# Performance work log

Hardware: AMD Instinct MI355X
Metric: run time of the kernel (lower is better)

## Reference

```python
import jax, jax.numpy as jnp
import numpy as np

B, H, P, L = 8, 512, 512, 2048
HIGH_STAB, LOW_STAB = 0.9, 0.99  # 0 <= high < |lambda| <= low <= 1 (discrete dynamics)


def setup_inputs() -> dict:
    key = jax.random.key(0)
    k_u, k_mag, k_ph, k_b, k_c, k_d = jax.random.split(key, 6)
    u = jax.random.normal(k_u, (B, H, L), dtype=jnp.float32)
    # Frozen diagonal reservoir state matrix Lambda_bar: complex eigenvalues with
    # magnitude in (high_stability, low_stability], random phase (stored as real/imag pairs).
    mag = jax.random.uniform(k_mag, (P,), minval=HIGH_STAB, maxval=LOW_STAB)
    phase = jax.random.uniform(k_ph, (P,), minval=0.0, maxval=2.0 * np.pi)
    Lambda_bar_ri = jnp.stack([mag * jnp.cos(phase), mag * jnp.sin(phase)], axis=-1)  # (P,2)
    B_bar_ri = jax.random.normal(k_b, (P, H, 2), dtype=jnp.float32)  # complex B_bar as real pairs
    C_ri = jax.random.normal(k_c, (H, P, 2), dtype=jnp.float32)      # complex C as real pairs
    D = jax.random.normal(k_d, (H, H), dtype=jnp.float32)
    return {"u": u, "Lambda_bar_ri": Lambda_bar_ri, "B_bar_ri": B_bar_ri, "C_ri": C_ri, "D": D}


def _binary_op(e_i, e_j):
    A_i, Bu_i = e_i
    A_j, Bu_j = e_j
    return (A_j * A_i, A_j * Bu_i + Bu_j)


def reference(u, Lambda_bar_ri, B_bar_ri, C_ri, D):
    Lam = jax.lax.complex(Lambda_bar_ri[:, 0], Lambda_bar_ri[:, 1])        # (P,)
    B_bar = jax.lax.complex(B_bar_ri[..., 0], B_bar_ri[..., 1])            # (P,H)
    C = jax.lax.complex(C_ri[..., 0], C_ri[..., 1])                        # (H,P)
    # Bu_t = B_bar @ u_t for all t, batched: (B,P,L) complex
    Bu = jnp.einsum('ph,bhl->bpl', B_bar, u.astype(B_bar.dtype))
    A = jnp.broadcast_to(Lam[None, :, None], Bu.shape)                     # (B,P,L)
    # Parallel associative scan: x_t = Lam * x_{t-1} + Bu_t
    _, x = jax.lax.associative_scan(_binary_op, (A, Bu), axis=2)           # (B,P,L)
    C_A_Bu = jnp.einsum('hp,bpl->bhl', C, x).real                          # (B,H,L)
    # torch.einsum('hh,bhl->bhl', D, u) uses only the diagonal of D
    Du = jnp.diagonal(D)[None, :, None] * u
    return jax.nn.gelu(C_A_Bu + Du, approximate=False)
```

## Files before the change

### kernel.cpp

```cpp
#include <hip/hip_runtime.h>
#include <cstdint>
#include <cstddef>

#define BB 8
#define HH 512
#define PP 512
#define LL 2048

typedef __attribute__((ext_vector_type(8))) __bf16 bf16x8;
typedef __attribute__((ext_vector_type(4))) float f32x4;

__device__ __forceinline__ uint16_t f2bf(float f) {
  uint32_t u = __builtin_bit_cast(uint32_t, f);
  u += 0x7FFFu + ((u >> 16) & 1u);
  return (uint16_t)(u >> 16);
}

__device__ __forceinline__ void async_copy16(const void* gptr, void* ldsptr) {
  __builtin_amdgcn_global_load_lds(
      (const __attribute__((address_space(1))) unsigned int*)gptr,
      (__attribute__((address_space(3))) unsigned int*)ldsptr,
      16, 0, 0);
}

__global__ __launch_bounds__(256) void prep_and_transpose(
    const float* __restrict__ U, const float* __restrict__ Bbar,
    const float* __restrict__ Cri, const float* __restrict__ Dm,
    uint16_t* __restrict__ Ut, uint16_t* __restrict__ A1,
    uint16_t* __restrict__ A2, float* __restrict__ Dd) {
  __shared__ uint16_t tile[64][66];
  const int t = threadIdx.x;
  if (blockIdx.x < 2048) {
    const int bid = blockIdx.x;
    const int b = bid >> 8;
    const int h0 = ((bid >> 5) & 7) * 64;
    const int l0 = (bid & 31) * 64;
    const int r = t >> 2, c = t & 3;
    const float* src = U + ((size_t)(b * 512 + h0 + r)) * 2048 + l0 + c * 16;
#pragma unroll
    for (int q = 0; q < 4; ++q) {
      float4 v = *(const float4*)(src + q * 4);
      *(uint32_t*)&tile[r][c * 16 + q * 4]     = (uint32_t)f2bf(v.x) | ((uint32_t)f2bf(v.y) << 16);
      *(uint32_t*)&tile[r][c * 16 + q * 4 + 2] = (uint32_t)f2bf(v.z) | ((uint32_t)f2bf(v.w) << 16);
    }
    __syncthreads();
    uint16_t* dst = Ut + ((size_t)(b * 2048 + l0 + r)) * 512 + h0 + c * 16;
    uint32_t o[8];
#pragma unroll
    for (int k = 0; k < 8; ++k)
      o[k] = (uint32_t)tile[c * 16 + 2 * k][r] | ((uint32_t)tile[c * 16 + 2 * k + 1][r] << 16);
    *(uint4*)(dst)     = make_uint4(o[0], o[1], o[2], o[3]);
    *(uint4*)(dst + 8) = make_uint4(o[4], o[5], o[6], o[7]);
  } else {
    int idx = (blockIdx.x - 2048) * 256 + t;
    int p = idx >> 9, h = idx & 511;
    A1[(size_t)p * 512 + h]          = f2bf(Bbar[((size_t)p * 512 + h) * 2 + 0]);
    A1[(size_t)(512 + p) * 512 + h]  = f2bf(Bbar[((size_t)p * 512 + h) * 2 + 1]);
    int h2 = idx >> 9, p2 = idx & 511;
    A2[(size_t)h2 * 1024 + p2]        = f2bf( Cri[((size_t)h2 * 512 + p2) * 2 + 0]);
    A2[(size_t)h2 * 1024 + 512 + p2]  = f2bf(-Cri[((size_t)h2 * 512 + p2) * 2 + 1]);
    if (idx < 512) Dd[idx] = Dm[(size_t)idx * 512 + idx];
  }
}

__global__ __launch_bounds__(512) void scan_tr(
    const float* __restrict__ Lam, const uint16_t* __restrict__ Bu,
    uint16_t* __restrict__ Xt8) {
  __shared__ uint16_t S[16][2048];
  const int t = threadIdx.x, wave = t >> 6, lane = t & 63;
  const int b = blockIdx.x >> 6, p0 = (blockIdx.x & 63) * 8, p = p0 + wave;

  const float lr = Lam[p * 2 + 0], li = Lam[p * 2 + 1];
  float ar = lr, ai = li;
#pragma unroll
  for (int s = 0; s < 5; ++s) { float nr = ar * ar - ai * ai, ni = 2.f * ar * ai; ar = nr; ai = ni; }

  const uint16_t* rowre = Bu + ((size_t)(b * 1024 + p)) * 2048 + lane * 32;
  const uint16_t* rowim = Bu + ((size_t)(b * 1024 + 512 + p)) * 2048 + lane * 32;
  uint4 vr[4], vi[4];
#pragma unroll
  for (int q = 0; q < 4; ++q) { vr[q] = ((const uint4*)rowre)[q]; vi[q] = ((const uint4*)rowim)[q]; }

  float xr[32], xi[32];
  float sr = 0.f, si = 0.f;
#pragma unroll
  for (int q = 0; q < 4; ++q) {
    uint32_t wr[4] = {vr[q].x, vr[q].y, vr[q].z, vr[q].w};
    uint32_t wi[4] = {vi[q].x, vi[q].y, vi[q].z, vi[q].w};
#pragma unroll
    for (int d = 0; d < 4; ++d) {
      float br0 = __builtin_bit_cast(float, wr[d] << 16);
      float bi0 = __builtin_bit_cast(float, wi[d] << 16);
      float br1 = __builtin_bit_cast(float, wr[d] & 0xFFFF0000u);
      float bi1 = __builtin_bit_cast(float, wi[d] & 0xFFFF0000u);
      int j = q * 8 + d * 2;
      float nr = lr * sr - li * si + br0, ni = lr * si + li * sr + bi0;
      sr = nr; si = ni; xr[j] = sr; xi[j] = si;
      nr = lr * sr - li * si + br1; ni = lr * si + li * sr + bi1;
      sr = nr; si = ni; xr[j + 1] = sr; xi[j + 1] = si;
    }
  }
  float Ar = ar, Ai = ai, Sr = sr, Si = si;
#pragma unroll
  for (int off = 1; off < 64; off <<= 1) {
    float pAr = __shfl_up(Ar, off), pAi = __shfl_up(Ai, off);
    float pSr = __shfl_up(Sr, off), pSi = __shfl_up(Si, off);
    if (lane >= off) {
      float tSr = Ar * pSr - Ai * pSi + Sr;
      float tSi = Ar * pSi + Ai * pSr + Si;
      float tAr = Ar * pAr - Ai * pAi;
      float tAi = Ar * pAi + Ai * pAr;
      Sr = tSr; Si = tSi; Ar = tAr; Ai = tAi;
    }
  }
  float Cr = __shfl_up(Sr, 1), Ci = __shfl_up(Si, 1);
  if (lane == 0) { Cr = 0.f; Ci = 0.f; }
  float fr_ = lr * Cr - li * Ci, fi_ = lr * Ci + li * Cr;
#pragma unroll
  for (int j = 0; j < 32; ++j) {
    xr[j] += fr_; xi[j] += fi_;
    float nfr = fr_ * lr - fi_ * li, nfi = fr_ * li + fi_ * lr;
    fr_ = nfr; fi_ = nfi;
  }
  const int wsw = (lane & 7) << 3;
#pragma unroll
  for (int q = 0; q < 4; ++q) {
    uint32_t wr[4], wi[4];
#pragma unroll
    for (int d = 0; d < 4; ++d) {
      int j = q * 8 + d * 2;
      wr[d] = (uint32_t)f2bf(xr[j]) | ((uint32_t)f2bf(xr[j + 1]) << 16);
      wi[d] = (uint32_t)f2bf(xi[j]) | ((uint32_t)f2bf(xi[j + 1]) << 16);
    }
    const int col = (lane * 32 + q * 8) ^ wsw;
    *(uint4*)&S[wave * 2 + 0][col] = make_uint4(wr[0], wr[1], wr[2], wr[3]);
    *(uint4*)&S[wave * 2 + 1][col] = make_uint4(wi[0], wi[1], wi[2], wi[3]);
  }
  __syncthreads();
  const size_t gre = (size_t)b * 128 + (p0 >> 3);
#pragma unroll
  for (int c = 0; c < 2; ++c) {
    uint16_t* dst = Xt8 + (gre + (size_t)c * 64) * 2048 * 8;
#pragma unroll
    for (int rep = 0; rep < 4; ++rep) {
      int l = rep * 512 + t;
      int ls = l ^ (((l >> 5) & 7) << 3);
      uint32_t o0 = (uint32_t)S[0 + c][ls] | ((uint32_t)S[2 + c][ls] << 16);
      uint32_t o1 = (uint32_t)S[4 + c][ls] | ((uint32_t)S[6 + c][ls] << 16);
      uint32_t o2 = (uint32_t)S[8 + c][ls] | ((uint32_t)S[10 + c][ls] << 16);
      uint32_t o3 = (uint32_t)S[12 + c][ls] | ((uint32_t)S[14 + c][ls] << 16);
      *(uint4*)(dst + (size_t)l * 8) = make_uint4(o0, o1, o2, o3);
    }
  }
}

#define GEMM_CORE(KDIM, PB0_EXPR, BSTRIDE)                                    \
  constexpr int K = (KDIM), NT = K / 32;                                      \
  __shared__ __align__(16) uint16_t Alds[2][128 * 32];                        \
  __shared__ __align__(16) uint16_t Blds[2][64 * 32];                         \
  const int t = threadIdx.x, lane = t & 63, w = t >> 6;                       \
  const int m0 = blockIdx.y * 128, n0 = blockIdx.x * 64, b = blockIdx.z;      \
  const int r0 = t >> 2;                                                      \
  const int c0 = (t & 3) ^ ((r0 >> 1) & 3);                                   \
  const uint16_t* pA0 = Amat + (size_t)(m0 + r0) * K + c0 * 8;                \
  const uint16_t* pA1 = Amat + (size_t)(m0 + 64 + r0) * K + c0 * 8;           \
  const uint16_t* pB0 = (PB0_EXPR);                                           \
  const int d0 = t * 8;                                                       \
  const int wm = (w >> 1) * 64, wn = (w & 1) * 32;                            \
  const int fr = lane & 15, fq = lane >> 4;                                   \
  int offA[4], offB[2];                                                       \
  _Pragma("unroll")                                                           \
  for (int i = 0; i < 4; ++i) {                                               \
    int rm = wm + i * 16 + fr;                                                \
    offA[i] = rm * 32 + ((fq ^ ((rm >> 1) & 3)) * 8);                         \
  }                                                                           \
  _Pragma("unroll")                                                           \
  for (int j = 0; j < 2; ++j) {                                               \
    int rn = wn + j * 16 + fr;                                                \
    offB[j] = rn * 32 + ((fq ^ ((rn >> 1) & 3)) * 8);                         \
  }                                                                           \
  f32x4 acc[4][2];                                                            \
  _Pragma("unroll")                                                           \
  for (int i = 0; i < 4; ++i)                                                 \
    _Pragma("unroll")                                                         \
    for (int j = 0; j < 2; ++j) acc[i][j] = (f32x4){0.f, 0.f, 0.f, 0.f};      \
  async_copy16(pA0, &Alds[0][d0]);                                            \
  async_copy16(pA1, &Alds[0][2048 + d0]);                                     \
  async_copy16(pB0, &Blds[0][d0]);                                            \
  __syncthreads();                                                            \
  _Pragma("unroll 2")                                                         \
  for (int it = 0; it < NT; ++it) {                                           \
    const int cur = it & 1, nxt = cur ^ 1;                                    \
    if (it + 1 < NT) {                                                        \
      const int kb = (it + 1) * 32;                                           \
      async_copy16(pA0 + kb, &Alds[nxt][d0]);                                 \
      async_copy16(pA1 + kb, &Alds[nxt][2048 + d0]);                          \
      async_copy16(pB0 + (size_t)(it + 1) * (BSTRIDE), &Blds[nxt][d0]);       \
    }                                                                         \
    bf16x8 af[4], bv[2];                                                      \
    _Pragma("unroll")                                                         \
    for (int i = 0; i < 4; ++i) af[i] = *(const bf16x8*)&Alds[cur][offA[i]];  \
    _Pragma("unroll")                                                         \
    for (int j = 0; j < 2; ++j) bv[j] = *(const bf16x8*)&Blds[cur][offB[j]];  \
    _Pragma("unroll")                                                         \
    for (int i = 0; i < 4; ++i)                                               \
      _Pragma("unroll")                                                       \
      for (int j = 0; j < 2; ++j)                                             \
        acc[i][j] = __builtin_amdgcn_mfma_f32_16x16x32_bf16(af[i], bv[j], acc[i][j], 0, 0, 0); \
    __syncthreads();                                                          \
  }

__global__ __launch_bounds__(256) void gemm1_fused(
    const uint16_t* __restrict__ Amat, const uint16_t* __restrict__ Bt,
    uint16_t* __restrict__ Bu) {
  GEMM_CORE(512, Bt + ((size_t)b * 2048 + n0 + r0) * 512 + c0 * 8, 32)
  uint16_t* O = Bu + ((size_t)b * 1024 + m0) * 2048 + n0;
#pragma unroll
  for (int i = 0; i < 4; ++i)
#pragma unroll
    for (int j = 0; j < 2; ++j)
#pragma unroll
      for (int r = 0; r < 4; ++r) {
        int mm = wm + i * 16 + fq * 4 + r;
        int nn = wn + j * 16 + fr;
        O[(size_t)mm * 2048 + nn] = f2bf(acc[i][j][r]);
      }
}

__global__ __launch_bounds__(256) void gemm2_fused(
    const uint16_t* __restrict__ Amat, const uint16_t* __restrict__ Bt,
    float* __restrict__ Out, const float* __restrict__ Dd,
    const float* __restrict__ Uu) {
  GEMM_CORE(1024, Bt + (((size_t)b * 128 + c0) * 2048 + n0 + r0) * 8, 65536)
  const size_t base = ((size_t)b * 512 + m0) * 2048 + n0;
  float* O = Out + base;
  const float* Ub = Uu + base;
#pragma unroll
  for (int i = 0; i < 4; ++i)
#pragma unroll
    for (int r = 0; r < 4; ++r) {
      int mm = wm + i * 16 + fq * 4 + r;
      float dv = Dd[m0 + mm];
#pragma unroll
      for (int j = 0; j < 2; ++j) {
        int nn = wn + j * 16 + fr;
        float xv = acc[i][j][r] + dv * Ub[(size_t)mm * 2048 + nn];
        O[(size_t)mm * 2048 + nn] = 0.5f * xv * (1.f + erff(xv * 0.70710678118654752f));
      }
    }
}

extern "C" void kernel_launch(void* const* d_in, const int* in_sizes, int n_in,
                              void* d_out, int out_size, void* d_ws, size_t ws_size,
                              hipStream_t stream) {
  const float* u    = (const float*)d_in[0];
  const float* Lam  = (const float*)d_in[1];
  const float* Bbar = (const float*)d_in[2];
  const float* Cri  = (const float*)d_in[3];
  const float* Dm   = (const float*)d_in[4];
  float* out = (float*)d_out;

  char* ws = (char*)d_ws;
  uint16_t* Bu  = (uint16_t*)(ws);
  uint16_t* Xt8 = (uint16_t*)(ws + 33554432);
  uint16_t* Ut  = (uint16_t*)(ws + 33554432);
  uint16_t* A1 = (uint16_t*)(ws + 67108864);
  uint16_t* A2 = (uint16_t*)(ws + 68157440);
  float*    Dd = (float*)   (ws + 69206016);

  prep_and_transpose<<<3072, 256, 0, stream>>>(u, Bbar, Cri, Dm, Ut, A1, A2, Dd);
  gemm1_fused<<<dim3(32, 8, BB), 256, 0, stream>>>(A1, Ut, Bu);
  scan_tr<<<512, 512, 0, stream>>>(Lam, Bu, Xt8);
  gemm2_fused<<<dim3(32, 4, BB), 256, 0, stream>>>(A2, Xt8, out, Dd, u);
}
```

Baseline: 173.2 us.

## Triple-buffer gemm2 LDS pipeline with explicit vmcnt waits and single barrier

The second GEMM moves from double buffering with two barriers per K step to a three-stage LDS ring. Loads are issued two tiles ahead, and explicit s_waitcnt vmcnt plus a single s_barrier per iteration replace the trailing __syncthreads. The goal is to hide global-to-LDS latency and cut barrier stalls. In exchange it uses more LDS per block, which may lower occupancy, and the loop is fully unrolled with hand-written waitcnt logic. The first GEMM is only restructured into the same macros and behaves as before.

```diff
diff --git a/kernel.cpp b/kernel.cpp
--- a/kernel.cpp
+++ b/kernel.cpp
@@ -154,10 +154,8 @@
   }
 }
 
-#define GEMM_CORE(KDIM, PB0_EXPR, BSTRIDE)                                    \
+#define GEMM_SETUP(KDIM, PB0_EXPR)                                            \
   constexpr int K = (KDIM), NT = K / 32;                                      \
-  __shared__ __align__(16) uint16_t Alds[2][128 * 32];                        \
-  __shared__ __align__(16) uint16_t Blds[2][64 * 32];                         \
   const int t = threadIdx.x, lane = t & 63, w = t >> 6;                       \
   const int m0 = blockIdx.y * 128, n0 = blockIdx.x * 64, b = blockIdx.z;      \
   const int r0 = t >> 2;                                                      \
@@ -183,37 +181,44 @@
   _Pragma("unroll")                                                           \
   for (int i = 0; i < 4; ++i)                                                 \
     _Pragma("unroll")                                                         \
-    for (int j = 0; j < 2; ++j) acc[i][j] = (f32x4){0.f, 0.f, 0.f, 0.f};      \
-  async_copy16(pA0, &Alds[0][d0]);                                            \
-  async_copy16(pA1, &Alds[0][2048 + d0]);                                     \
-  async_copy16(pB0, &Blds[0][d0]);                                            \
-  __syncthreads();                                                            \
-  _Pragma("unroll 2")                                                         \
-  for (int it = 0; it < NT; ++it) {                                           \
-    const int cur = it & 1, nxt = cur ^ 1;                                    \
-    if (it + 1 < NT) {                                                        \
-      const int kb = (it + 1) * 32;                                           \
-      async_copy16(pA0 + kb, &Alds[nxt][d0]);                                 \
-      async_copy16(pA1 + kb, &Alds[nxt][2048 + d0]);                          \
-      async_copy16(pB0 + (size_t)(it + 1) * (BSTRIDE), &Blds[nxt][d0]);       \
-    }                                                                         \
+    for (int j = 0; j < 2; ++j) acc[i][j] = (f32x4){0.f, 0.f, 0.f, 0.f};
+
+#define GEMM_MFMA_BLOCK(BUF_A, BUF_B)                                         \
+  {                                                                           \
     bf16x8 af[4], bv[2];                                                      \
     _Pragma("unroll")                                                         \
-    for (int i = 0; i < 4; ++i) af[i] = *(const bf16x8*)&Alds[cur][offA[i]];  \
+    for (int i = 0; i < 4; ++i) af[i] = *(const bf16x8*)&(BUF_A)[offA[i]];    \
     _Pragma("unroll")                                                         \
-    for (int j = 0; j < 2; ++j) bv[j] = *(const bf16x8*)&Blds[cur][offB[j]];  \
+    for (int j = 0; j < 2; ++j) bv[j] = *(const bf16x8*)&(BUF_B)[offB[j]];    \
     _Pragma("unroll")                                                         \
     for (int i = 0; i < 4; ++i)                                               \
       _Pragma("unroll")                                                       \
       for (int j = 0; j < 2; ++j)                                             \
         acc[i][j] = __builtin_amdgcn_mfma_f32_16x16x32_bf16(af[i], bv[j], acc[i][j], 0, 0, 0); \
-    __syncthreads();                                                          \
   }
 
 __global__ __launch_bounds__(256) void gemm1_fused(
     const uint16_t* __restrict__ Amat, const uint16_t* __restrict__ Bt,
     uint16_t* __restrict__ Bu) {
-  GEMM_CORE(512, Bt + ((size_t)b * 2048 + n0 + r0) * 512 + c0 * 8, 32)
+  __shared__ __align__(16) uint16_t Alds[2][128 * 32];
+  __shared__ __align__(16) uint16_t Blds[2][64 * 32];
+  GEMM_SETUP(512, Bt + ((size_t)b * 2048 + n0 + r0) * 512 + c0 * 8)
+  async_copy16(pA0, &Alds[0][d0]);
+  async_copy16(pA1, &Alds[0][2048 + d0]);
+  async_copy16(pB0, &Blds[0][d0]);
+  __syncthreads();
+#pragma unroll 2
+  for (int it = 0; it < NT; ++it) {
+    const int cur = it & 1, nxt = cur ^ 1;
+    if (it + 1 < NT) {
+      const int kb = (it + 1) * 32;
+      async_copy16(pA0 + kb, &Alds[nxt][d0]);
+      async_copy16(pA1 + kb, &Alds[nxt][2048 + d0]);
+      async_copy16(pB0 + kb, &Blds[nxt][d0]);
+    }
+    GEMM_MFMA_BLOCK(Alds[cur], Blds[cur])
+    __syncthreads();
+  }
   uint16_t* O = Bu + ((size_t)b * 1024 + m0) * 2048 + n0;
 #pragma unroll
   for (int i = 0; i < 4; ++i)
@@ -231,7 +236,32 @@
     const uint16_t* __restrict__ Amat, const uint16_t* __restrict__ Bt,
     float* __restrict__ Out, const float* __restrict__ Dd,
     const float* __restrict__ Uu) {
-  GEMM_CORE(1024, Bt + (((size_t)b * 128 + c0) * 2048 + n0 + r0) * 8, 65536)
+  __shared__ __align__(16) uint16_t Alds[3][128 * 32];
+  __shared__ __align__(16) uint16_t Blds[3][64 * 32];
+  GEMM_SETUP(1024, Bt + (((size_t)b * 128 + c0) * 2048 + n0 + r0) * 8)
+  constexpr size_t BSTRIDE = 65536;
+  async_copy16(pA0,           &Alds[0][d0]);
+  async_copy16(pA1,           &Alds[0][2048 + d0]);
+  async_copy16(pB0,           &Blds[0][d0]);
+  async_copy16(pA0 + 32,      &Alds[1][d0]);
+  async_copy16(pA1 + 32,      &Alds[1][2048 + d0]);
+  async_copy16(pB0 + BSTRIDE, &Blds[1][d0]);
+#pragma unroll
+  for (int kt = 0; kt < NT; ++kt) {
+    const int cur = kt % 3;
+    if (kt + 1 < NT) asm volatile("s_waitcnt vmcnt(3)" ::: "memory");
+    else             asm volatile("s_waitcnt vmcnt(0)" ::: "memory");
+    __builtin_amdgcn_s_barrier();
+    __builtin_amdgcn_sched_barrier(0);
+    if (kt + 2 < NT) {
+      const int nb = (kt + 2) % 3;
+      const int kb = (kt + 2) * 32;
+      async_copy16(pA0 + kb, &Alds[nb][d0]);
+      async_copy16(pA1 + kb, &Alds[nb][2048 + d0]);
+      async_copy16(pB0 + (size_t)(kt + 2) * BSTRIDE, &Blds[nb][d0]);
+    }
+    GEMM_MFMA_BLOCK(Alds[cur], Blds[cur])
+  }
   const size_t base = ((size_t)b * 512 + m0) * 2048 + n0;
   float* O = Out + base;
   const float* Ub = Uu + base;
```

After: 174.4 us. About the same (+0.7%).
